# Performance work log

Measured on AMD Instinct MI355X. Metric: run time of the kernel, lower is better.

The kernel has to match this reference:

```python
import jax, jax.numpy as jnp
import numpy as np

G, NPG, HC, LAT, FF, EDIM, EH = 8, 4096, 16, 64, 512, 3, 64
N = G * NPG            # 32768 total nodes
E = 393216             # avg degree 12


def setup_inputs() -> dict:
    key = jax.random.key(0)
    ks = jax.random.split(key, 16)
    w = lambda k, s: jax.random.normal(k, s, jnp.float32) * 0.02
    inp = {
        "x": jax.random.normal(ks[0], (G, LAT), jnp.float32),
        "edge_index": jax.random.randint(ks[1], (2, E), 0, N, dtype=jnp.int64),
        "edge_attr": jax.random.normal(ks[2], (E, EDIM), jnp.float32),
        "fc2_w": w(ks[3], (LAT, FF)),   "fc2_b": jnp.zeros((FF,), jnp.float32),
        "fc1_w": w(ks[4], (FF, NPG * HC)), "fc1_b": jnp.zeros((NPG * HC,), jnp.float32),
    }
    for i in range(2):
        inp[f"conv{i}_root"] = w(ks[5 + 4 * i], (HC, HC))
        inp[f"conv{i}_bias"] = jnp.zeros((HC,), jnp.float32)
        inp[f"conv{i}_w1"] = w(ks[6 + 4 * i], (EDIM, EH))
        inp[f"conv{i}_b1"] = jnp.zeros((EH,), jnp.float32)
        inp[f"conv{i}_w2"] = w(ks[7 + 4 * i], (EH, HC * HC))
        inp[f"conv{i}_b2"] = jnp.zeros((HC * HC,), jnp.float32)
    return inp


def _nnconv(x, src, dst, ea, root, bias, w1, b1, w2, b2):
    # edge-conditioned conv (NNConv): per-edge weight matrix from edge MLP
    theta = (jax.nn.relu(ea @ w1 + b1) @ w2 + b2).reshape(-1, HC, HC)  # [E,HC,HC]
    msg = jnp.einsum('ei,eio->eo', x[src], theta)                       # gather+per-edge matvec
    aggr = jax.ops.segment_sum(msg, dst, num_segments=N)                # scatter-add
    return x @ root + aggr + bias


def reference(x, edge_index, edge_attr, fc2_w, fc2_b, fc1_w, fc1_b,
              conv0_root, conv0_bias, conv0_w1, conv0_b1, conv0_w2, conv0_b2,
              conv1_root, conv1_bias, conv1_w1, conv1_b1, conv1_w2, conv1_b2):
    h = x @ fc2_w + fc2_b                      # [G, FF]
    h = jax.nn.elu(h @ fc1_w + fc1_b)          # [G, NPG*HC]
    h = h.reshape(N, HC)                       # node features
    src, dst = edge_index[0], edge_index[1]
    convs = ((conv0_root, conv0_bias, conv0_w1, conv0_b1, conv0_w2, conv0_b2),
             (conv1_root, conv1_bias, conv1_w1, conv1_b1, conv1_w2, conv1_b2))
    for (root, b, w1, b1, w2, b2) in convs:
        h = jax.nn.elu(_nnconv(h, src, dst, edge_attr, root, b, w1, b1, w2, b2))
        # dropout is identity in eval mode
    return h
```

## Files before the change

### kernel.cpp

```cpp
#include <hip/hip_runtime.h>
#include <math.h>

#define G_   8
#define NPG_ 4096
#define HC_  16
#define LAT_ 64
#define FF_  512
#define EDIM_ 3
#define EH_  64
#define NN_  32768
#define EE_  393216

__global__ void k_front1(const float* __restrict__ x, const float* __restrict__ w,
                         const float* __restrict__ b, float* __restrict__ h1) {
  int c = blockIdx.x * blockDim.x + threadIdx.x;
  if (c >= FF_) return;
  float acc[G_];
#pragma unroll
  for (int g = 0; g < G_; g++) acc[g] = 0.f;
  for (int r = 0; r < LAT_; r++) {
    float wv = w[r * FF_ + c];
#pragma unroll
    for (int g = 0; g < G_; g++) acc[g] = fmaf(x[g * LAT_ + r], wv, acc[g]);
  }
#pragma unroll
  for (int g = 0; g < G_; g++) h1[g * FF_ + c] = acc[g] + b[c];
}

__global__ __launch_bounds__(512) void k_front2(const float* __restrict__ h1,
                                                const float* __restrict__ w,
                                                const float* __restrict__ b,
                                                float* __restrict__ hn) {
  __shared__ float sh[G_ * FF_];
  for (int i = threadIdx.x; i < G_ * FF_; i += blockDim.x) sh[i] = h1[i];
  __syncthreads();
  int g = threadIdx.x >> 6;
  int lane = threadIdx.x & 63;
  int c = blockIdx.x * 64 + lane;
  const float* shg = &sh[g * FF_];
  float acc = 0.f;
#pragma unroll 8
  for (int r = 0; r < FF_; r++) acc = fmaf(shg[r], w[r * (NPG_ * HC_) + c], acc);
  float v = acc + b[c];
  hn[g * (NPG_ * HC_) + c] = v > 0.f ? v : expm1f(v);
}

__global__ void k_zero(int* __restrict__ p, int nv) {
  int i = blockIdx.x * blockDim.x + threadIdx.x;
  if (i < nv) p[i] = 0;
}
__global__ void k_hist(const int* __restrict__ key, int* __restrict__ cnt) {
  int e = blockIdx.x * blockDim.x + threadIdx.x;
  if (e < EE_) atomicAdd(&cnt[key[e]], 1);
}
__global__ __launch_bounds__(1024) void k_scan(const int* __restrict__ cnt,
                                               int* __restrict__ rowptr,
                                               int* __restrict__ cursor) {
  __shared__ int part[1024];
  int t = threadIdx.x;
  int base = t * 32;
  int loc[32];
  int s = 0;
#pragma unroll
  for (int i = 0; i < 32; i++) { loc[i] = s; s += cnt[base + i]; }
  part[t] = s;
  __syncthreads();
  for (int off = 1; off < 1024; off <<= 1) {
    int v = (t >= off) ? part[t - off] : 0;
    __syncthreads();
    part[t] += v;
    __syncthreads();
  }
  int pre = (t == 0) ? 0 : part[t - 1];
#pragma unroll
  for (int i = 0; i < 32; i++) {
    int v = pre + loc[i];
    rowptr[base + i] = v;
    cursor[base + i] = v;
  }
  if (t == 1023) rowptr[NN_] = part[1023];
}
__global__ void k_scatter(const int* __restrict__ src, int* __restrict__ cursor,
                          int* __restrict__ perm) {
  int e = blockIdx.x * blockDim.x + threadIdx.x;
  if (e < EE_) {
    int pos = atomicAdd(&cursor[src[e]], 1);
    perm[pos] = e;
  }
}

__global__ void k_gather(const int* __restrict__ perm, const int* __restrict__ dst,
                         const float* __restrict__ ea, float4* __restrict__ eas4) {
  int e = blockIdx.x * blockDim.x + threadIdx.x;
  if (e >= EE_ + 8) return;
  float4 v = make_float4(0.f, 0.f, 0.f, __int_as_float(0));
  if (e < EE_) {
    int eid = perm[e];
    v.x = ea[eid * 3];
    v.y = ea[eid * 3 + 1];
    v.z = ea[eid * 3 + 2];
    v.w = __int_as_float(dst[eid]);
  }
  eas4[e] = v;
}

__global__ void k_nodeinit(const float* __restrict__ hn, const float* __restrict__ root,
                           const float* __restrict__ bias, float* __restrict__ out) {
  int idx = blockIdx.x * blockDim.x + threadIdx.x;
  if (idx >= NN_ * HC_) return;
  int nd = idx >> 4, o = idx & 15;
  float acc = bias[o];
#pragma unroll
  for (int i = 0; i < 16; i++) acc = fmaf(hn[nd * 16 + i], root[i * 16 + o], acc);
  out[idx] = acc;
}

__global__ void k_wprep(const float* __restrict__ w2, const float* __restrict__ w1,
                        const float* __restrict__ b1, float* __restrict__ W2m,
                        float4* __restrict__ w1p4) {
  int idx = blockIdx.x * 256 + threadIdx.x;
  if (idx < 16384) {
    int i  = idx >> 10;
    int j4 = (idx >> 8) & 3;
    int l  = (idx >> 2) & 63;
    int c  = idx & 3;
    int q = l >> 4, o = l & 15;
    int h = q * 16 + j4 * 4 + c;
    W2m[idx] = w2[h * 256 + i * 16 + o];
  }
  if (idx < 64) {
    w1p4[idx] = make_float4(w1[idx], w1[64 + idx], w1[128 + idx], b1[idx]);
  }
}

__global__ __launch_bounds__(256, 4) void k_precM(
    const float* __restrict__ hn, const float* __restrict__ W2m,
    float4* __restrict__ Mbuf4, int n0base) {
  int tid = threadIdx.x;
  int wave = tid >> 6, l = tid & 63;
  int n0 = n0base + (blockIdx.x * 4 + wave) * 4;
  const float4* __restrict__ W2m4 = (const float4*)W2m;

  float4 a0[4], a1[4], a2[4], a3[4];
#pragma unroll
  for (int j4 = 0; j4 < 4; j4++) {
    a0[j4] = make_float4(0.f, 0.f, 0.f, 0.f);
    a1[j4] = make_float4(0.f, 0.f, 0.f, 0.f);
    a2[j4] = make_float4(0.f, 0.f, 0.f, 0.f);
    a3[j4] = make_float4(0.f, 0.f, 0.f, 0.f);
  }
  for (int i = 0; i < 16; i++) {
    float x0 = hn[(n0 + 0) * 16 + i];
    float x1 = hn[(n0 + 1) * 16 + i];
    float x2 = hn[(n0 + 2) * 16 + i];
    float x3 = hn[(n0 + 3) * 16 + i];
#pragma unroll
    for (int j4 = 0; j4 < 4; j4++) {
      float4 w = W2m4[i * 256 + j4 * 64 + l];
      a0[j4].x = fmaf(x0, w.x, a0[j4].x); a0[j4].y = fmaf(x0, w.y, a0[j4].y);
      a0[j4].z = fmaf(x0, w.z, a0[j4].z); a0[j4].w = fmaf(x0, w.w, a0[j4].w);
      a1[j4].x = fmaf(x1, w.x, a1[j4].x); a1[j4].y = fmaf(x1, w.y, a1[j4].y);
      a1[j4].z = fmaf(x1, w.z, a1[j4].z); a1[j4].w = fmaf(x1, w.w, a1[j4].w);
      a2[j4].x = fmaf(x2, w.x, a2[j4].x); a2[j4].y = fmaf(x2, w.y, a2[j4].y);
      a2[j4].z = fmaf(x2, w.z, a2[j4].z); a2[j4].w = fmaf(x2, w.w, a2[j4].w);
      a3[j4].x = fmaf(x3, w.x, a3[j4].x); a3[j4].y = fmaf(x3, w.y, a3[j4].y);
      a3[j4].z = fmaf(x3, w.z, a3[j4].z); a3[j4].w = fmaf(x3, w.w, a3[j4].w);
    }
  }
  int s0 = (n0 - n0base) * 256;
#pragma unroll
  for (int j4 = 0; j4 < 4; j4++) Mbuf4[s0 + j4 * 64 + l] = a0[j4];
#pragma unroll
  for (int j4 = 0; j4 < 4; j4++) Mbuf4[s0 + 256 + j4 * 64 + l] = a1[j4];
#pragma unroll
  for (int j4 = 0; j4 < 4; j4++) Mbuf4[s0 + 512 + j4 * 64 + l] = a2[j4];
#pragma unroll
  for (int j4 = 0; j4 < 4; j4++) Mbuf4[s0 + 768 + j4 * 64 + l] = a3[j4];
}

__global__ __launch_bounds__(256, 4) void k_edge(
    const float* __restrict__ hn, const int* __restrict__ rowptr,
    const float4* __restrict__ eas4, const float4* __restrict__ w1p4,
    const float* __restrict__ b2, const float4* __restrict__ Mbuf4,
    float* __restrict__ hnext, int n0base) {
  int tid = threadIdx.x;
  int wave = tid >> 6, l = tid & 63;
  int o = l & 15, q = l >> 4;
  int n = n0base + blockIdx.x * 4 + wave;

  int rs = rowptr[n], re = rowptr[n + 1];
  if (rs >= re) return;

  int mb = (n - n0base) * 256 + l;
  float4 m0 = Mbuf4[mb], m1 = Mbuf4[mb + 64], m2 = Mbuf4[mb + 128],
         m3 = Mbuf4[mb + 192];
  float M[16] = {m0.x, m0.y, m0.z, m0.w, m1.x, m1.y, m1.z, m1.w,
                 m2.x, m2.y, m2.z, m2.w, m3.x, m3.y, m3.z, m3.w};

  const float4* __restrict__ hx4 = (const float4*)&hn[n * 16];
  float T = 0.f;
#pragma unroll
  for (int i4 = 0; i4 < 4; i4++) {
    float4 xq = hx4[i4];
    T = fmaf(xq.x, b2[(i4 * 4 + 0) * 16 + o], T);
    T = fmaf(xq.y, b2[(i4 * 4 + 1) * 16 + o], T);
    T = fmaf(xq.z, b2[(i4 * 4 + 2) * 16 + o], T);
    T = fmaf(xq.w, b2[(i4 * 4 + 3) * 16 + o], T);
  }

  const float4* __restrict__ w1v = &w1p4[q * 16];

  float4 c0 = eas4[rs], c1 = eas4[rs + 1], c2 = eas4[rs + 2], c3 = eas4[rs + 3];
  for (int k = rs; k < re; k += 4) {
    float4 n0 = eas4[k + 4], n1 = eas4[k + 5], n2 = eas4[k + 6], n3 = eas4[k + 7];

    float p0 = 0.f, p1 = 0.f, p2 = 0.f, p3 = 0.f;
#pragma unroll
    for (int j = 0; j < 16; j++) {
      float4 wv = w1v[j];
      float m = M[j];
      float h0 = fmaxf(fmaf(c0.z, wv.z, fmaf(c0.y, wv.y, fmaf(c0.x, wv.x, wv.w))), 0.f);
      float h1 = fmaxf(fmaf(c1.z, wv.z, fmaf(c1.y, wv.y, fmaf(c1.x, wv.x, wv.w))), 0.f);
      float h2 = fmaxf(fmaf(c2.z, wv.z, fmaf(c2.y, wv.y, fmaf(c2.x, wv.x, wv.w))), 0.f);
      float h3 = fmaxf(fmaf(c3.z, wv.z, fmaf(c3.y, wv.y, fmaf(c3.x, wv.x, wv.w))), 0.f);
      p0 = fmaf(h0, m, p0);
      p1 = fmaf(h1, m, p1);
      p2 = fmaf(h2, m, p2);
      p3 = fmaf(h3, m, p3);
    }
    p0 += __shfl_xor(p0, 16); p1 += __shfl_xor(p1, 16);
    p2 += __shfl_xor(p2, 16); p3 += __shfl_xor(p3, 16);
    p0 += __shfl_xor(p0, 32); p1 += __shfl_xor(p1, 32);
    p2 += __shfl_xor(p2, 32); p3 += __shfl_xor(p3, 32);

    float vv  = (q == 0) ? p0   : (q == 1) ? p1   : (q == 2) ? p2   : p3;
    float dpf = (q == 0) ? c0.w : (q == 1) ? c1.w : (q == 2) ? c2.w : c3.w;
    if (k + q < re) atomicAdd(&hnext[__float_as_int(dpf) * 16 + o], vv + T);

    c0 = n0; c1 = n1; c2 = n2; c3 = n3;
  }
}

__global__ void k_elu(const float* __restrict__ in, float* __restrict__ out) {
  int idx = blockIdx.x * blockDim.x + threadIdx.x;
  if (idx >= NN_ * HC_) return;
  float v = in[idx];
  out[idx] = v > 0.f ? v : expm1f(v);
}

extern "C" void kernel_launch(void* const* d_in, const int* in_sizes, int n_in,
                              void* d_out, int out_size, void* d_ws, size_t ws_size,
                              hipStream_t stream) {
  const float* x    = (const float*)d_in[0];
  const int*   ei   = (const int*)d_in[1];
  const float* ea   = (const float*)d_in[2];
  const float* fc2w = (const float*)d_in[3];
  const float* fc2b = (const float*)d_in[4];
  const float* fc1w = (const float*)d_in[5];
  const float* fc1b = (const float*)d_in[6];
  float* out = (float*)d_out;

  const size_t MBUF_FULL = (size_t)NN_ * 1024;
  size_t fixed = 4096 + 2 * (size_t)NN_ * HC_ + 16384 + 256 +
                 (size_t)(EE_ + 8) * 4;
  size_t ints  = (size_t)NN_ * 3 + 1 + EE_;
  int chunk = ((fixed + MBUF_FULL + ints) * 4 + 1024 <= ws_size) ? NN_ : 8192;

  float* ws = (float*)d_ws;
  float*  h1     = ws;
  float*  hnode  = h1 + 4096;
  float*  hnext  = hnode + (size_t)NN_ * HC_;
  float*  W2m    = hnext + (size_t)NN_ * HC_;
  float4* w1p4   = (float4*)(W2m + 16384);
  float4* eas4   = (float4*)(W2m + 16384 + 256);
  float4* Mbuf4  = (float4*)(W2m + 16384 + 256 + (size_t)(EE_ + 8) * 4);
  int*    cnt    = (int*)((float*)Mbuf4 + (size_t)chunk * 1024);
  int*    rowptr = cnt + NN_;
  int*    cursor = rowptr + NN_ + 1;
  int*    perm   = cursor + NN_;

  const int* src  = ei;
  const int* dstp = ei + EE_;

  k_front1<<<2, 256, 0, stream>>>(x, fc2w, fc2b, h1);
  k_front2<<<1024, 512, 0, stream>>>(h1, fc1w, fc1b, hnode);

  k_zero<<<(NN_ + 255) / 256, 256, 0, stream>>>(cnt, NN_);
  k_hist<<<(EE_ + 255) / 256, 256, 0, stream>>>(src, cnt);
  k_scan<<<1, 1024, 0, stream>>>(cnt, rowptr, cursor);
  k_scatter<<<(EE_ + 255) / 256, 256, 0, stream>>>(src, cursor, perm);
  k_gather<<<(EE_ + 8 + 255) / 256, 256, 0, stream>>>(perm, dstp, ea, eas4);

  for (int cv = 0; cv < 2; cv++) {
    const float* root = (const float*)d_in[7 + cv * 6];
    const float* cb   = (const float*)d_in[8 + cv * 6];
    const float* w1   = (const float*)d_in[9 + cv * 6];
    const float* b1   = (const float*)d_in[10 + cv * 6];
    const float* w2   = (const float*)d_in[11 + cv * 6];
    const float* b2   = (const float*)d_in[12 + cv * 6];
    k_wprep<<<64, 256, 0, stream>>>(w2, w1, b1, W2m, w1p4);
    k_nodeinit<<<NN_ * HC_ / 256, 256, 0, stream>>>(hnode, root, cb, hnext);
    for (int c = 0; c < NN_ / chunk; c++) {
      k_precM<<<chunk / 16, 256, 0, stream>>>(hnode, W2m, Mbuf4, c * chunk);
      k_edge<<<chunk / 4, 256, 0, stream>>>(hnode, rowptr, eas4, w1p4, b2,
                                            Mbuf4, hnext, c * chunk);
    }
    k_elu<<<NN_ * HC_ / 256, 256, 0, stream>>>(hnext, cv == 0 ? hnode : out);
  }
}
```

Baseline: 376.3 us.

## Interleave edge pairs for packed FP32 FMA and fuse scatter with gather

```diff
diff --git a/kernel.cpp b/kernel.cpp
--- a/kernel.cpp
+++ b/kernel.cpp
@@ -10,6 +10,26 @@
 #define EH_  64
 #define NN_  32768
 #define EE_  393216
+#define EPAD_ (EE_ + NN_ + 8)
+
+typedef float v2f __attribute__((ext_vector_type(2)));
+typedef float v4f __attribute__((ext_vector_type(4)));
+
+#if __has_builtin(__builtin_elementwise_fma) && __has_builtin(__builtin_elementwise_max)
+static __device__ __forceinline__ v2f pkfma2(v2f a, v2f b, v2f c) {
+  return __builtin_elementwise_fma(a, b, c);
+}
+static __device__ __forceinline__ v2f pkmax2(v2f a, v2f b) {
+  return __builtin_elementwise_max(a, b);
+}
+#else
+static __device__ __forceinline__ v2f pkfma2(v2f a, v2f b, v2f c) {
+  v2f r; r.x = fmaf(a.x, b.x, c.x); r.y = fmaf(a.y, b.y, c.y); return r;
+}
+static __device__ __forceinline__ v2f pkmax2(v2f a, v2f b) {
+  v2f r; r.x = fmaxf(a.x, b.x); r.y = fmaxf(a.y, b.y); return r;
+}
+#endif
 
 __global__ void k_front1(const float* __restrict__ x, const float* __restrict__ w,
                          const float* __restrict__ b, float* __restrict__ h1) {
@@ -62,7 +82,10 @@
   int loc[32];
   int s = 0;
 #pragma unroll
-  for (int i = 0; i < 32; i++) { loc[i] = s; s += cnt[base + i]; }
+  for (int i = 0; i < 32; i++) {
+    loc[i] = s;
+    s += (cnt[base + i] + 1) & ~1;
+  }
   part[t] = s;
   __syncthreads();
   for (int off = 1; off < 1024; off <<= 1) {
@@ -80,28 +103,24 @@
   }
   if (t == 1023) rowptr[NN_] = part[1023];
 }
-__global__ void k_scatter(const int* __restrict__ src, int* __restrict__ cursor,
-                          int* __restrict__ perm) {
+__global__ void k_pfill(float4* __restrict__ pairb) {
+  int p = blockIdx.x * blockDim.x + threadIdx.x;
+  if (p >= EPAD_ / 2) return;
+  float df = __int_as_float(NN_);
+  pairb[p * 2]     = make_float4(0.f, 0.f, 0.f, 0.f);
+  pairb[p * 2 + 1] = make_float4(0.f, 0.f, df, df);
+}
+__global__ void k_scatter(const int* __restrict__ src, const int* __restrict__ dst,
+                          const float* __restrict__ ea, int* __restrict__ cursor,
+                          float* __restrict__ pairb) {
   int e = blockIdx.x * blockDim.x + threadIdx.x;
-  if (e < EE_) {
-    int pos = atomicAdd(&cursor[src[e]], 1);
-    perm[pos] = e;
-  }
-}
-
-__global__ void k_gather(const int* __restrict__ perm, const int* __restrict__ dst,
-                         const float* __restrict__ ea, float4* __restrict__ eas4) {
-  int e = blockIdx.x * blockDim.x + threadIdx.x;
-  if (e >= EE_ + 8) return;
-  float4 v = make_float4(0.f, 0.f, 0.f, __int_as_float(0));
-  if (e < EE_) {
-    int eid = perm[e];
-    v.x = ea[eid * 3];
-    v.y = ea[eid * 3 + 1];
-    v.z = ea[eid * 3 + 2];
-    v.w = __int_as_float(dst[eid]);
-  }
-  eas4[e] = v;
+  if (e >= EE_) return;
+  int pos = atomicAdd(&cursor[src[e]], 1);
+  int b = (pos >> 1) * 8 + (pos & 1);
+  pairb[b]     = ea[e * 3];
+  pairb[b + 2] = ea[e * 3 + 1];
+  pairb[b + 4] = ea[e * 3 + 2];
+  pairb[b + 6] = __int_as_float(dst[e]);
 }
 
 __global__ void k_nodeinit(const float* __restrict__ hn, const float* __restrict__ root,
@@ -135,10 +154,10 @@
 
 __global__ __launch_bounds__(256, 4) void k_precM(
     const float* __restrict__ hn, const float* __restrict__ W2m,
-    float4* __restrict__ Mbuf4, int n0base) {
+    float4* __restrict__ Mbuf4) {
   int tid = threadIdx.x;
   int wave = tid >> 6, l = tid & 63;
-  int n0 = n0base + (blockIdx.x * 4 + wave) * 4;
+  int n0 = (blockIdx.x * 4 + wave) * 4;
   const float4* __restrict__ W2m4 = (const float4*)W2m;
 
   float4 a0[4], a1[4], a2[4], a3[4];
@@ -167,7 +186,7 @@
       a3[j4].z = fmaf(x3, w.z, a3[j4].z); a3[j4].w = fmaf(x3, w.w, a3[j4].w);
     }
   }
-  int s0 = (n0 - n0base) * 256;
+  int s0 = n0 * 256;
 #pragma unroll
   for (int j4 = 0; j4 < 4; j4++) Mbuf4[s0 + j4 * 64 + l] = a0[j4];
 #pragma unroll
@@ -180,18 +199,18 @@
 
 __global__ __launch_bounds__(256, 4) void k_edge(
     const float* __restrict__ hn, const int* __restrict__ rowptr,
-    const float4* __restrict__ eas4, const float4* __restrict__ w1p4,
+    const v4f* __restrict__ pairb, const float4* __restrict__ w1p4,
     const float* __restrict__ b2, const float4* __restrict__ Mbuf4,
-    float* __restrict__ hnext, int n0base) {
+    float* __restrict__ hnext) {
   int tid = threadIdx.x;
   int wave = tid >> 6, l = tid & 63;
   int o = l & 15, q = l >> 4;
-  int n = n0base + blockIdx.x * 4 + wave;
+  int n = blockIdx.x * 4 + wave;
 
   int rs = rowptr[n], re = rowptr[n + 1];
   if (rs >= re) return;
 
-  int mb = (n - n0base) * 256 + l;
+  int mb = n * 256 + l;
   float4 m0 = Mbuf4[mb], m1 = Mbuf4[mb + 64], m2 = Mbuf4[mb + 128],
          m3 = Mbuf4[mb + 192];
   float M[16] = {m0.x, m0.y, m0.z, m0.w, m1.x, m1.y, m1.z, m1.w,
@@ -210,31 +229,39 @@
 
   const float4* __restrict__ w1v = &w1p4[q * 16];
 
-  float4 c0 = eas4[rs], c1 = eas4[rs + 1], c2 = eas4[rs + 2], c3 = eas4[rs + 3];
+  v4f c0 = pairb[rs], c1 = pairb[rs + 1], c2 = pairb[rs + 2], c3 = pairb[rs + 3];
   for (int k = rs; k < re; k += 4) {
-    float4 n0 = eas4[k + 4], n1 = eas4[k + 5], n2 = eas4[k + 6], n3 = eas4[k + 7];
-
-    float p0 = 0.f, p1 = 0.f, p2 = 0.f, p3 = 0.f;
+    v4f n0 = pairb[k + 4], n1 = pairb[k + 5], n2 = pairb[k + 6], n3 = pairb[k + 7];
+
+    v2f eXa = __builtin_shufflevector(c0, c0, 0, 1);
+    v2f eYa = __builtin_shufflevector(c0, c0, 2, 3);
+    v2f eZa = __builtin_shufflevector(c1, c1, 0, 1);
+    v2f eXb = __builtin_shufflevector(c2, c2, 0, 1);
+    v2f eYb = __builtin_shufflevector(c2, c2, 2, 3);
+    v2f eZb = __builtin_shufflevector(c3, c3, 0, 1);
+    v2f pA = {0.f, 0.f}, pB = {0.f, 0.f};
+    v2f z2 = {0.f, 0.f};
 #pragma unroll
     for (int j = 0; j < 16; j++) {
       float4 wv = w1v[j];
-      float m = M[j];
-      float h0 = fmaxf(fmaf(c0.z, wv.z, fmaf(c0.y, wv.y, fmaf(c0.x, wv.x, wv.w))), 0.f);
-      float h1 = fmaxf(fmaf(c1.z, wv.z, fmaf(c1.y, wv.y, fmaf(c1.x, wv.x, wv.w))), 0.f);
-      float h2 = fmaxf(fmaf(c2.z, wv.z, fmaf(c2.y, wv.y, fmaf(c2.x, wv.x, wv.w))), 0.f);
-      float h3 = fmaxf(fmaf(c3.z, wv.z, fmaf(c3.y, wv.y, fmaf(c3.x, wv.x, wv.w))), 0.f);
-      p0 = fmaf(h0, m, p0);
-      p1 = fmaf(h1, m, p1);
-      p2 = fmaf(h2, m, p2);
-      p3 = fmaf(h3, m, p3);
+      v2f wx = {wv.x, wv.x};
+      v2f wy = {wv.y, wv.y};
+      v2f wz = {wv.z, wv.z};
+      v2f wc = {wv.w, wv.w};
+      v2f m2v = {M[j], M[j]};
+      v2f hA = pkmax2(pkfma2(eZa, wz, pkfma2(eYa, wy, pkfma2(eXa, wx, wc))), z2);
+      v2f hB = pkmax2(pkfma2(eZb, wz, pkfma2(eYb, wy, pkfma2(eXb, wx, wc))), z2);
+      pA = pkfma2(hA, m2v, pA);
+      pB = pkfma2(hB, m2v, pB);
     }
+    float p0 = pA.x, p1 = pA.y, p2 = pB.x, p3 = pB.y;
     p0 += __shfl_xor(p0, 16); p1 += __shfl_xor(p1, 16);
     p2 += __shfl_xor(p2, 16); p3 += __shfl_xor(p3, 16);
     p0 += __shfl_xor(p0, 32); p1 += __shfl_xor(p1, 32);
     p2 += __shfl_xor(p2, 32); p3 += __shfl_xor(p3, 32);
 
-    float vv  = (q == 0) ? p0   : (q == 1) ? p1   : (q == 2) ? p2   : p3;
-    float dpf = (q == 0) ? c0.w : (q == 1) ? c1.w : (q == 2) ? c2.w : c3.w;
+    float vv  = (q == 0) ? p0 : (q == 1) ? p1 : (q == 2) ? p2 : p3;
+    float dpf = (q == 0) ? c1[2] : (q == 1) ? c1[3] : (q == 2) ? c3[2] : c3[3];
     if (k + q < re) atomicAdd(&hnext[__float_as_int(dpf) * 16 + o], vv + T);
 
     c0 = n0; c1 = n1; c2 = n2; c3 = n3;
@@ -260,24 +287,17 @@
   const float* fc1b = (const float*)d_in[6];
   float* out = (float*)d_out;
 
-  const size_t MBUF_FULL = (size_t)NN_ * 1024;
-  size_t fixed = 4096 + 2 * (size_t)NN_ * HC_ + 16384 + 256 +
-                 (size_t)(EE_ + 8) * 4;
-  size_t ints  = (size_t)NN_ * 3 + 1 + EE_;
-  int chunk = ((fixed + MBUF_FULL + ints) * 4 + 1024 <= ws_size) ? NN_ : 8192;
-
   float* ws = (float*)d_ws;
   float*  h1     = ws;
   float*  hnode  = h1 + 4096;
   float*  hnext  = hnode + (size_t)NN_ * HC_;
-  float*  W2m    = hnext + (size_t)NN_ * HC_;
+  float*  W2m    = hnext + (size_t)NN_ * HC_ + 16;
   float4* w1p4   = (float4*)(W2m + 16384);
-  float4* eas4   = (float4*)(W2m + 16384 + 256);
-  float4* Mbuf4  = (float4*)(W2m + 16384 + 256 + (size_t)(EE_ + 8) * 4);
-  int*    cnt    = (int*)((float*)Mbuf4 + (size_t)chunk * 1024);
+  float*  pairb  = (float*)w1p4 + 256;
+  float4* Mbuf4  = (float4*)(pairb + (size_t)EPAD_ * 4);
+  int*    cnt    = (int*)((float*)Mbuf4 + (size_t)NN_ * 1024);
   int*    rowptr = cnt + NN_;
   int*    cursor = rowptr + NN_ + 1;
-  int*    perm   = cursor + NN_;
 
   const int* src  = ei;
   const int* dstp = ei + EE_;
@@ -288,8 +308,8 @@
   k_zero<<<(NN_ + 255) / 256, 256, 0, stream>>>(cnt, NN_);
   k_hist<<<(EE_ + 255) / 256, 256, 0, stream>>>(src, cnt);
   k_scan<<<1, 1024, 0, stream>>>(cnt, rowptr, cursor);
-  k_scatter<<<(EE_ + 255) / 256, 256, 0, stream>>>(src, cursor, perm);
-  k_gather<<<(EE_ + 8 + 255) / 256, 256, 0, stream>>>(perm, dstp, ea, eas4);
+  k_pfill<<<(EPAD_ / 2 + 255) / 256, 256, 0, stream>>>((float4*)pairb);
+  k_scatter<<<(EE_ + 255) / 256, 256, 0, stream>>>(src, dstp, ea, cursor, pairb);
 
   for (int cv = 0; cv < 2; cv++) {
     const float* root = (const float*)d_in[7 + cv * 6];
@@ -300,11 +320,9 @@
     const float* b2   = (const float*)d_in[12 + cv * 6];
     k_wprep<<<64, 256, 0, stream>>>(w2, w1, b1, W2m, w1p4);
     k_nodeinit<<<NN_ * HC_ / 256, 256, 0, stream>>>(hnode, root, cb, hnext);
-    for (int c = 0; c < NN_ / chunk; c++) {
-      k_precM<<<chunk / 16, 256, 0, stream>>>(hnode, W2m, Mbuf4, c * chunk);
-      k_edge<<<chunk / 4, 256, 0, stream>>>(hnode, rowptr, eas4, w1p4, b2,
-                                            Mbuf4, hnext, c * chunk);
-    }
+    k_precM<<<NN_ / 16, 256, 0, stream>>>(hnode, W2m, Mbuf4);
+    k_edge<<<NN_ / 4, 256, 0, stream>>>(hnode, rowptr, (const v4f*)pairb, w1p4,
+                                        b2, Mbuf4, hnext);
     k_elu<<<NN_ * HC_ / 256, 256, 0, stream>>>(hnext, cv == 0 ? hnode : out);
   }
 }
```

After: 1.277 ms. +239.4%, slower.
